# Optimization experiments

Measured on AMD Instinct MI355X. Metric: run time of the kernel, lower is better.

The kernel has to match this reference:

```python
import jax, jax.numpy as jnp
import numpy as np

N = 100000      # num nodes (in_features)
E = 1600000     # num edges
P = 100000      # num pos/neg label edges
EMB = 64        # embedding dim (hardcoded 64 in Encoder)
HID = 128       # 2 * out_channels
OUT = 64        # out_channels
EPS = 1e-15     # PyG GAE EPS
MAX_LOGSTD = 10.0


def setup_inputs() -> dict:
    key = jax.random.key(0)
    ks = jax.random.split(key, 10)
    emb_weight = jax.random.normal(ks[0], (N, EMB), dtype=jnp.float32) * 0.1
    edge_index = jax.random.randint(ks[1], (2, E), 0, N, dtype=jnp.int64)
    pos_edge_label_index = jax.random.randint(ks[2], (2, P), 0, N, dtype=jnp.int64)
    neg_edge_label_index = jax.random.randint(ks[3], (2, P), 0, N, dtype=jnp.int64)
    W1 = jax.random.normal(ks[4], (EMB, HID), dtype=jnp.float32) / np.sqrt(EMB)
    b1 = jnp.zeros((HID,), dtype=jnp.float32)
    W_mu = jax.random.normal(ks[5], (HID, OUT), dtype=jnp.float32) / np.sqrt(HID)
    b_mu = jnp.zeros((OUT,), dtype=jnp.float32)
    W_ls = jax.random.normal(ks[6], (HID, OUT), dtype=jnp.float32) / np.sqrt(HID)
    b_ls = jnp.zeros((OUT,), dtype=jnp.float32)
    return {
        'emb_weight': emb_weight, 'edge_index': edge_index,
        'W1': W1, 'b1': b1, 'W_mu': W_mu, 'b_mu': b_mu, 'W_ls': W_ls, 'b_ls': b_ls,
        'pos_edge_label_index': pos_edge_label_index,
        'neg_edge_label_index': neg_edge_label_index,
    }


def gcn_conv(x, src, dst, deg_inv_sqrt, W, b):
    # GCNConv with added self-loops and symmetric normalization:
    # out = D^{-1/2} (A + I) D^{-1/2} (x W) + b
    h = x @ W                                  # [N, F_out]
    norm = deg_inv_sqrt[src] * deg_inv_sqrt[dst]          # [E]
    agg = jax.ops.segment_sum(h[src] * norm[:, None], dst, num_segments=N)
    agg = agg + h * (deg_inv_sqrt * deg_inv_sqrt)[:, None]  # self-loop term
    return agg + b


def reference(emb_weight, edge_index, W1, b1, W_mu, b_mu, W_ls, b_ls,
              pos_edge_label_index, neg_edge_label_index):
    src, dst = edge_index[0], edge_index[1]
    # degree includes self-loop weight 1
    deg = jax.ops.segment_sum(jnp.ones((E,), dtype=emb_weight.dtype), dst, num_segments=N) + 1.0
    deg_inv_sqrt = jax.lax.rsqrt(deg)

    h = jax.nn.relu(gcn_conv(emb_weight, src, dst, deg_inv_sqrt, W1, b1))
    mu = gcn_conv(h, src, dst, deg_inv_sqrt, W_mu, b_mu)
    logstd = jnp.minimum(gcn_conv(h, src, dst, deg_inv_sqrt, W_ls, b_ls), MAX_LOGSTD)
    z = mu  # eval-mode reparametrize returns mu

    # recon_loss: inner-product decoder + BCE on pos/neg label edges
    ps, pd = pos_edge_label_index[0], pos_edge_label_index[1]
    ns, nd = neg_edge_label_index[0], neg_edge_label_index[1]
    pos_p = jax.nn.sigmoid(jnp.sum(z[ps] * z[pd], axis=-1))
    neg_p = jax.nn.sigmoid(jnp.sum(z[ns] * z[nd], axis=-1))
    pos_loss = -jnp.mean(jnp.log(pos_p + EPS))
    neg_loss = -jnp.mean(jnp.log(1.0 - neg_p + EPS))
    loss = pos_loss + neg_loss
    return z, logstd, loss
```

## Files before the change

kernel.cpp:

```cpp
#include <hip/hip_runtime.h>
#include <hip/hip_bf16.h>
#include <hip/hip_fp16.h>

#define NN 100000
#define NE 1600000
#define NP 100000

typedef _Float16 h2v __attribute__((ext_vector_type(2)));

__device__ __forceinline__ float fdot2u(uint a, uint b, float c) {
    union { uint u; h2v h; } ua, ub;
    ua.u = a; ub.u = b;
    return __builtin_amdgcn_fdot2(ua.h, ub.h, c, false);
}

__device__ __forceinline__ uint packh2(float lo, float hi) {
    __half2 h = __floats2half2_rn(lo, hi);
    return *(uint*)&h;
}

__device__ __forceinline__ void h8_to_f(const uint4 u, float* f) {
    const __half2* hp = (const __half2*)&u;
    float2 t0 = __half22float2(hp[0]), t1 = __half22float2(hp[1]);
    float2 t2 = __half22float2(hp[2]), t3 = __half22float2(hp[3]);
    f[0] = t0.x; f[1] = t0.y; f[2] = t1.x; f[3] = t1.y;
    f[4] = t2.x; f[5] = t2.y; f[6] = t3.x; f[7] = t3.y;
}

__device__ __forceinline__ void add8(const uint4 u, float* acc) {
    float f[8]; h8_to_f(u, f);
#pragma unroll
    for (int i = 0; i < 8; ++i) acc[i] += f[i];
}

__device__ __forceinline__ uint4 f_to_h8(const float* f) {
    union { __half2 h[4]; uint4 u; } pk;
    pk.h[0] = __floats2half2_rn(f[0], f[1]);
    pk.h[1] = __floats2half2_rn(f[2], f[3]);
    pk.h[2] = __floats2half2_rn(f[4], f[5]);
    pk.h[3] = __floats2half2_rn(f[6], f[7]);
    return pk.u;
}

#define RNG 400
#define NBK 250
#define K_A 8000
#define CAPB 12288

__global__ __launch_bounds__(256) void k_hist(const int* __restrict__ ei,
                                              int* __restrict__ bcnt) {
    __shared__ int hist[NBK];
    int tid = threadIdx.x;
    int e0 = blockIdx.x * K_A;
    for (int i = tid; i < NBK; i += 256) hist[i] = 0;
    __syncthreads();
    for (int i = tid; i < K_A; i += 256) atomicAdd(&hist[ei[NE + e0 + i] / RNG], 1);
    __syncthreads();
    for (int i = tid; i < NBK; i += 256) if (hist[i]) atomicAdd(&bcnt[i], hist[i]);
}

__global__ __launch_bounds__(256) void k_bscan(const int* __restrict__ bcnt,
                                               int* __restrict__ bbase,
                                               int* __restrict__ gcnt) {
    __shared__ int c[NBK];
    int tid = threadIdx.x;
    if (tid < NBK) c[tid] = bcnt[tid];
    __syncthreads();
    if (tid < 64) {
        int run = 0;
        for (int g = 0; g < NBK; g += 64) {
            int idx = g + tid;
            int v = (idx < NBK) ? c[idx] : 0;
            int inc = v;
#pragma unroll
            for (int off = 1; off < 64; off <<= 1) {
                int t2 = __shfl_up(inc, off);
                if (tid >= off) inc += t2;
            }
            if (idx < NBK) { int ex = run + inc - v; bbase[idx] = ex; gcnt[idx] = ex; }
            run += __shfl(inc, 63);
        }
        if (tid == 0) bbase[NBK] = run;
    }
}

__global__ __launch_bounds__(256) void k_binA(const int* __restrict__ ei,
                                              int* __restrict__ gcnt,
                                              int* __restrict__ edges) {
    __shared__ int buf[K_A];
    __shared__ int hist[NBK], lofs[NBK + 1], lcnt[NBK], gbase[NBK];
    int tid = threadIdx.x;
    int e0 = blockIdx.x * K_A;
    for (int i = tid; i < NBK; i += 256) { hist[i] = 0; lcnt[i] = 0; }
    __syncthreads();
    for (int i = tid; i < K_A; i += 256) atomicAdd(&hist[ei[NE + e0 + i] / RNG], 1);
    __syncthreads();
    if (tid < 64) {
        int run = 0;
        for (int g = 0; g < NBK; g += 64) {
            int idx = g + tid;
            int v = (idx < NBK) ? hist[idx] : 0;
            int inc = v;
#pragma unroll
            for (int off = 1; off < 64; off <<= 1) {
                int t2 = __shfl_up(inc, off);
                if (tid >= off) inc += t2;
            }
            if (idx < NBK) lofs[idx] = run + inc - v;
            run += __shfl(inc, 63);
        }
        if (tid == 0) lofs[NBK] = run;
    }
    for (int i = tid; i < NBK; i += 256) gbase[i] = atomicAdd(&gcnt[i], hist[i]);
    __syncthreads();
    for (int i = tid; i < K_A; i += 256) {
        int s = ei[e0 + i], d = ei[NE + e0 + i];
        int b = d / RNG;
        int dl = d - b * RNG;
        int p = lofs[b] + atomicAdd(&lcnt[b], 1);
        buf[p] = s | (dl << 17);
    }
    __syncthreads();
    for (int j = tid; j < K_A; j += 256) {
        int loB = 0, hiB = NBK;
        while (hiB - loB > 1) {
            int mid = (loB + hiB) >> 1;
            if (lofs[mid] <= j) loB = mid; else hiB = mid;
        }
        edges[gbase[loB] + (j - lofs[loB])] = buf[j];
    }
}

__global__ __launch_bounds__(256) void k_binB(const int* __restrict__ bbase,
                                              int* __restrict__ edges,
                                              int* __restrict__ rowptr,
                                              float* __restrict__ dinv) {
    __shared__ int buf[CAPB];
    __shared__ int hist[RNG], lrp[RNG], lcnt[RNG];
    int tid = threadIdx.x;
    int b = blockIdx.x;
    int lo = b * RNG;
    int base = bbase[b], n = bbase[b + 1] - base;
    for (int i = tid; i < RNG; i += 256) { hist[i] = 0; lcnt[i] = 0; }
    __syncthreads();
    for (int i = tid; i < n; i += 256)
        atomicAdd(&hist[((unsigned)edges[base + i]) >> 17], 1);
    __syncthreads();
    if (tid < 64) {
        int run = 0;
        for (int g = 0; g < RNG; g += 64) {
            int idx = g + tid;
            int v = (idx < RNG) ? hist[idx] : 0;
            int inc = v;
#pragma unroll
            for (int off = 1; off < 64; off <<= 1) {
                int t2 = __shfl_up(inc, off);
                if (tid >= off) inc += t2;
            }
            if (idx < RNG) lrp[idx] = run + inc - v;
            run += __shfl(inc, 63);
        }
    }
    __syncthreads();
    for (int i = tid; i < RNG; i += 256) {
        dinv[lo + i] = rsqrtf((float)hist[i] + 1.0f);
        rowptr[lo + i] = base + lrp[i];
    }
    if (b == NBK - 1 && tid == 0) rowptr[NN] = base + n;
    int ovS0 = -1, ovS1 = -1, ovR0 = 0, ovR1 = 0;
    for (int i = tid; i < n; i += 256) {
        int rec = edges[base + i];
        int dl = ((unsigned)rec) >> 17;
        int src = rec & 0x1FFFF;
        int slot = lrp[dl] + atomicAdd(&lcnt[dl], 1);
        if (slot < CAPB) buf[slot] = src;
        else if (ovS0 < 0) { ovS0 = slot; ovR0 = src; }
        else { ovS1 = slot; ovR1 = src; }
    }
    __syncthreads();
    int lim = n < CAPB ? n : CAPB;
    for (int i = tid; i < lim; i += 256) edges[base + i] = buf[i];
    if (ovS0 >= 0) edges[base + ovS0] = ovR0;
    if (ovS1 >= 0) edges[base + ovS1] = ovR1;
}

__global__ void k_cvt(const float4* __restrict__ in4, const float* __restrict__ dinv,
                      uint4* __restrict__ out) {
    int t = blockIdx.x * blockDim.x + threadIdx.x;
    if (t >= NN * 8) return;
    float dv = dinv[t >> 3];
    float4 a = in4[t * 2], b = in4[t * 2 + 1];
    float f[8] = {a.x * dv, a.y * dv, a.z * dv, a.w * dv,
                  b.x * dv, b.y * dv, b.z * dv, b.w * dv};
    out[t] = f_to_h8(f);
}

__global__ __launch_bounds__(512) void k_l1(const uint4* __restrict__ x16,
                                            const float* __restrict__ dinv,
                                            const int* __restrict__ rowptr,
                                            const int* __restrict__ edges,
                                            const float4* __restrict__ W1_4,
                                            const float* __restrict__ b1,
                                            uint2* __restrict__ h16) {
    __shared__ uint4 w16h[32 * 32];
    __shared__ uint rows16[64 * 32];
    __shared__ float sdinv[64];
    int t = threadIdx.x;
    int base = blockIdx.x * 64;
#pragma unroll
    for (int i = 0; i < 2; ++i) {
        int idx = t + i * 512;
        int kp = idx >> 5, jg = idx & 31;
        float4 we = W1_4[(2 * kp) * 32 + jg];
        float4 wo = W1_4[(2 * kp + 1) * 32 + jg];
        w16h[idx] = make_uint4(packh2(we.x, wo.x), packh2(we.y, wo.y),
                               packh2(we.z, wo.z), packh2(we.w, wo.w));
    }
    if (t < 64) sdinv[t] = (base + t < NN) ? dinv[base + t] : 0.0f;
    int rl = t >> 3, q = t & 7;
    int r = base + rl;
    if (r < NN) {
        float acc[8];
        h8_to_f(x16[(size_t)r * 8 + q], acc);
        int j = rowptr[r], j1 = rowptr[r + 1];
        for (; j + 8 <= j1; j += 8) {
            int e[8]; uint4 v[8];
#pragma unroll
            for (int i = 0; i < 8; ++i) e[i] = edges[j + i];
#pragma unroll
            for (int i = 0; i < 8; ++i) v[i] = x16[(size_t)e[i] * 8 + q];
#pragma unroll
            for (int i = 0; i < 8; ++i) add8(v[i], acc);
        }
        if (j + 4 <= j1) {
            int e[4]; uint4 v[4];
#pragma unroll
            for (int i = 0; i < 4; ++i) e[i] = edges[j + i];
#pragma unroll
            for (int i = 0; i < 4; ++i) v[i] = x16[(size_t)e[i] * 8 + q];
#pragma unroll
            for (int i = 0; i < 4; ++i) add8(v[i], acc);
            j += 4;
        }
        for (; j < j1; ++j) add8(x16[(size_t)edges[j] * 8 + q], acc);
        float dr = dinv[r];
#pragma unroll
        for (int i = 0; i < 8; ++i) acc[i] *= dr;
#pragma unroll
        for (int i = 0; i < 4; ++i)
            rows16[rl * 32 + 4 * q + i] = packh2(acc[2 * i], acc[2 * i + 1]);
    }
    __syncthreads();
    int rg = t >> 5, jg = t & 31;
    int r0 = rg * 4;
    float4 bias = ((const float4*)b1)[jg];
    float acc[4][4];
#pragma unroll
    for (int r2 = 0; r2 < 4; ++r2) {
        acc[r2][0] = bias.x; acc[r2][1] = bias.y; acc[r2][2] = bias.z; acc[r2][3] = bias.w;
    }
#pragma unroll 4
    for (int kp = 0; kp < 32; ++kp) {
        uint f0 = rows16[(r0 + 0) * 32 + kp];
        uint f1 = rows16[(r0 + 1) * 32 + kp];
        uint f2 = rows16[(r0 + 2) * 32 + kp];
        uint f3 = rows16[(r0 + 3) * 32 + kp];
        uint4 wv = w16h[kp * 32 + jg];
        acc[0][0] = fdot2u(f0, wv.x, acc[0][0]); acc[0][1] = fdot2u(f0, wv.y, acc[0][1]);
        acc[0][2] = fdot2u(f0, wv.z, acc[0][2]); acc[0][3] = fdot2u(f0, wv.w, acc[0][3]);
        acc[1][0] = fdot2u(f1, wv.x, acc[1][0]); acc[1][1] = fdot2u(f1, wv.y, acc[1][1]);
        acc[1][2] = fdot2u(f1, wv.z, acc[1][2]); acc[1][3] = fdot2u(f1, wv.w, acc[1][3]);
        acc[2][0] = fdot2u(f2, wv.x, acc[2][0]); acc[2][1] = fdot2u(f2, wv.y, acc[2][1]);
        acc[2][2] = fdot2u(f2, wv.z, acc[2][2]); acc[2][3] = fdot2u(f2, wv.w, acc[2][3]);
        acc[3][0] = fdot2u(f3, wv.x, acc[3][0]); acc[3][1] = fdot2u(f3, wv.y, acc[3][1]);
        acc[3][2] = fdot2u(f3, wv.z, acc[3][2]); acc[3][3] = fdot2u(f3, wv.w, acc[3][3]);
    }
#pragma unroll
    for (int r2 = 0; r2 < 4; ++r2) {
        int row = base + r0 + r2;
        if (row < NN) {
            float dv = sdinv[r0 + r2];
            union { __half2 h[2]; uint2 u; } pk;
            pk.h[0] = __floats2half2_rn(fmaxf(acc[r2][0], 0.0f) * dv,
                                        fmaxf(acc[r2][1], 0.0f) * dv);
            pk.h[1] = __floats2half2_rn(fmaxf(acc[r2][2], 0.0f) * dv,
                                        fmaxf(acc[r2][3], 0.0f) * dv);
            h16[(size_t)row * 32 + jg] = pk.u;
        }
    }
}

__global__ __launch_bounds__(512) void k_l2(const uint4* __restrict__ x16,
                                            const float* __restrict__ dinv,
                                            const int* __restrict__ rowptr,
                                            const int* __restrict__ edges,
                                            const float4* __restrict__ Wmu4,
                                            const float* __restrict__ bmu,
                                            const float4* __restrict__ Wls4,
                                            const float* __restrict__ bls,
                                            float* __restrict__ out,
                                            uint2* __restrict__ z16) {
    __shared__ uint4 w16h[64 * 32];
    __shared__ uint rows16[64 * 64];
    int t = threadIdx.x;
    int base = blockIdx.x * 64;
#pragma unroll
    for (int i = 0; i < 4; ++i) {
        int idx = t + i * 512;
        int kp = idx >> 5, jg = idx & 31;
        int jj = (jg < 16) ? jg : (jg - 16);
        const float4* W = (jg < 16) ? Wmu4 : Wls4;
        float4 we = W[(2 * kp) * 16 + jj];
        float4 wo = W[(2 * kp + 1) * 16 + jj];
        w16h[idx] = make_uint4(packh2(we.x, wo.x), packh2(we.y, wo.y),
                               packh2(we.z, wo.z), packh2(we.w, wo.w));
    }
    int rl = t >> 3, q = t & 7;
    int r = base + rl;
    if (r < NN) {
        float acc[16];
        {
            uint4 s0 = x16[(size_t)r * 16 + 2 * q];
            uint4 s1 = x16[(size_t)r * 16 + 2 * q + 1];
            h8_to_f(s0, acc); h8_to_f(s1, acc + 8);
        }
        int j = rowptr[r], j1 = rowptr[r + 1];
        for (; j + 4 <= j1; j += 4) {
            int e[4]; uint4 va[4], vb[4];
#pragma unroll
            for (int i = 0; i < 4; ++i) e[i] = edges[j + i];
#pragma unroll
            for (int i = 0; i < 4; ++i) {
                va[i] = x16[(size_t)e[i] * 16 + 2 * q];
                vb[i] = x16[(size_t)e[i] * 16 + 2 * q + 1];
            }
#pragma unroll
            for (int i = 0; i < 4; ++i) { add8(va[i], acc); add8(vb[i], acc + 8); }
        }
        for (; j < j1; ++j) {
            int e = edges[j];
            add8(x16[(size_t)e * 16 + 2 * q], acc);
            add8(x16[(size_t)e * 16 + 2 * q + 1], acc + 8);
        }
        float dr = dinv[r];
#pragma unroll
        for (int i = 0; i < 16; ++i) acc[i] *= dr;
#pragma unroll
        for (int i = 0; i < 8; ++i)
            rows16[rl * 64 + 8 * q + i] = packh2(acc[2 * i], acc[2 * i + 1]);
    }
    __syncthreads();
    int rg = t >> 5, jg = t & 31;
    int r0 = rg * 4;
    float4 bias = (jg < 16) ? ((const float4*)bmu)[jg] : ((const float4*)bls)[jg - 16];
    float acc[4][4];
#pragma unroll
    for (int r2 = 0; r2 < 4; ++r2) {
        acc[r2][0] = bias.x; acc[r2][1] = bias.y; acc[r2][2] = bias.z; acc[r2][3] = bias.w;
    }
#pragma unroll 4
    for (int kp = 0; kp < 64; ++kp) {
        uint f0 = rows16[(r0 + 0) * 64 + kp];
        uint f1 = rows16[(r0 + 1) * 64 + kp];
        uint f2 = rows16[(r0 + 2) * 64 + kp];
        uint f3 = rows16[(r0 + 3) * 64 + kp];
        uint4 wv = w16h[kp * 32 + jg];
        acc[0][0] = fdot2u(f0, wv.x, acc[0][0]); acc[0][1] = fdot2u(f0, wv.y, acc[0][1]);
        acc[0][2] = fdot2u(f0, wv.z, acc[0][2]); acc[0][3] = fdot2u(f0, wv.w, acc[0][3]);
        acc[1][0] = fdot2u(f1, wv.x, acc[1][0]); acc[1][1] = fdot2u(f1, wv.y, acc[1][1]);
        acc[1][2] = fdot2u(f1, wv.z, acc[1][2]); acc[1][3] = fdot2u(f1, wv.w, acc[1][3]);
        acc[2][0] = fdot2u(f2, wv.x, acc[2][0]); acc[2][1] = fdot2u(f2, wv.y, acc[2][1]);
        acc[2][2] = fdot2u(f2, wv.z, acc[2][2]); acc[2][3] = fdot2u(f2, wv.w, acc[2][3]);
        acc[3][0] = fdot2u(f3, wv.x, acc[3][0]); acc[3][1] = fdot2u(f3, wv.y, acc[3][1]);
        acc[3][2] = fdot2u(f3, wv.z, acc[3][2]); acc[3][3] = fdot2u(f3, wv.w, acc[3][3]);
    }
    float4* out4 = (float4*)out;
    if (jg < 16) {
#pragma unroll
        for (int r2 = 0; r2 < 4; ++r2) {
            int row = base + r0 + r2;
            if (row < NN) {
                out4[(size_t)row * 16 + jg] =
                    make_float4(acc[r2][0], acc[r2][1], acc[r2][2], acc[r2][3]);
                union { __half2 h[2]; uint2 u; } pk;
                pk.h[0] = __floats2half2_rn(acc[r2][0], acc[r2][1]);
                pk.h[1] = __floats2half2_rn(acc[r2][2], acc[r2][3]);
                z16[(size_t)row * 16 + jg] = pk.u;
            }
        }
    } else {
#pragma unroll
        for (int r2 = 0; r2 < 4; ++r2) {
            int row = base + r0 + r2;
            if (row < NN) {
                float4 o = make_float4(fminf(acc[r2][0], 10.0f), fminf(acc[r2][1], 10.0f),
                                       fminf(acc[r2][2], 10.0f), fminf(acc[r2][3], 10.0f));
                out4[(size_t)NN * 16 + (size_t)row * 16 + (jg - 16)] = o;
            }
        }
    }
}

__global__ __launch_bounds__(256) void k_loss(const int* __restrict__ pos,
                                              const int* __restrict__ neg,
                                              const uint2* __restrict__ z16,
                                              float* __restrict__ accum) {
    int t = blockIdx.x * blockDim.x + threadIdx.x;
    int grp = t >> 4, q = t & 15;
    int e0 = grp * 4;
    bool isNeg = e0 >= NP;
    const int* idx = isNeg ? neg : pos;
    int eb = isNeg ? e0 - NP : e0;
    int a0 = idx[eb + 0], b0 = idx[NP + eb + 0];
    int a1 = idx[eb + 1], b1 = idx[NP + eb + 1];
    int a2 = idx[eb + 2], b2 = idx[NP + eb + 2];
    int a3 = idx[eb + 3], b3 = idx[NP + eb + 3];
    uint2 ua0 = z16[(size_t)a0 * 16 + q], ub0 = z16[(size_t)b0 * 16 + q];
    uint2 ua1 = z16[(size_t)a1 * 16 + q], ub1 = z16[(size_t)b1 * 16 + q];
    uint2 ua2 = z16[(size_t)a2 * 16 + q], ub2 = z16[(size_t)b2 * 16 + q];
    uint2 ua3 = z16[(size_t)a3 * 16 + q], ub3 = z16[(size_t)b3 * 16 + q];
    float d0 = fdot2u(ua0.y, ub0.y, fdot2u(ua0.x, ub0.x, 0.0f));
    float d1 = fdot2u(ua1.y, ub1.y, fdot2u(ua1.x, ub1.x, 0.0f));
    float d2 = fdot2u(ua2.y, ub2.y, fdot2u(ua2.x, ub2.x, 0.0f));
    float d3 = fdot2u(ua3.y, ub3.y, fdot2u(ua3.x, ub3.x, 0.0f));
#pragma unroll
    for (int off = 1; off < 16; off <<= 1) {
        d0 += __shfl_xor(d0, off);
        d1 += __shfl_xor(d1, off);
        d2 += __shfl_xor(d2, off);
        d3 += __shfl_xor(d3, off);
    }
    __shared__ float bsum[2];
    if (threadIdx.x < 2) bsum[threadIdx.x] = 0.0f;
    __syncthreads();
    if (q == 0) {
        float term;
        if (isNeg) {
            term = logf(1.0f - 1.0f / (1.0f + expf(-d0)) + 1e-15f)
                 + logf(1.0f - 1.0f / (1.0f + expf(-d1)) + 1e-15f)
                 + logf(1.0f - 1.0f / (1.0f + expf(-d2)) + 1e-15f)
                 + logf(1.0f - 1.0f / (1.0f + expf(-d3)) + 1e-15f);
        } else {
            term = logf(1.0f / (1.0f + expf(-d0)) + 1e-15f)
                 + logf(1.0f / (1.0f + expf(-d1)) + 1e-15f)
                 + logf(1.0f / (1.0f + expf(-d2)) + 1e-15f)
                 + logf(1.0f / (1.0f + expf(-d3)) + 1e-15f);
        }
        atomicAdd(&bsum[isNeg ? 1 : 0], term);
    }
    __syncthreads();
    if (threadIdx.x < 2) atomicAdd(&accum[threadIdx.x], bsum[threadIdx.x]);
}

__global__ void k_fin(const float* __restrict__ accum, float* __restrict__ out) {
    out[(size_t)NN * 128] = -(accum[0] + accum[1]) * (1.0f / (float)NP);
}

extern "C" void kernel_launch(void* const* d_in, const int* in_sizes, int n_in,
                              void* d_out, int out_size, void* d_ws, size_t ws_size,
                              hipStream_t stream) {
    const float* emb = (const float*)d_in[0];
    const int*   ei  = (const int*)d_in[1];
    const float* W1  = (const float*)d_in[2];
    const float* b1  = (const float*)d_in[3];
    const float* Wmu = (const float*)d_in[4];
    const float* bmu = (const float*)d_in[5];
    const float* Wls = (const float*)d_in[6];
    const float* bls = (const float*)d_in[7];
    const int*   pos = (const int*)d_in[8];
    const int*   neg = (const int*)d_in[9];
    float* out = (float*)d_out;

    char* ws = (char*)d_ws;
    float* dinv   = (float*)(ws);
    int*   rowptr = (int*)  (ws + (512 << 10));
    int*   bcnt   = (int*)  (ws + (1024 << 10));
    int*   bbase  = (int*)  (ws + (1028 << 10));
    int*   gcnt   = (int*)  (ws + (1032 << 10));
    float* accum  = (float*)(ws + (1040 << 10));
    const size_t OFF_EDGES = (2048 << 10);
    const size_t OFF_H16   = OFF_EDGES + (size_t)NE * 4;
    const size_t OFF_E16   = OFF_H16 + (size_t)NN * 128 * 2;
    int*   edges  = (int*)(ws + OFF_EDGES);
    uint2* h16    = (uint2*)(ws + OFF_H16);
    uint4* emb16  = (uint4*)(ws + OFF_E16);
    uint2* z16    = (uint2*)(ws + OFF_E16);

    hipMemsetAsync(bcnt, 0, NBK * sizeof(int), stream);
    hipMemsetAsync(accum, 0, 2 * sizeof(float), stream);

    k_hist <<<NE / K_A, 256, 0, stream>>>(ei, bcnt);
    k_bscan<<<1, 256, 0, stream>>>(bcnt, bbase, gcnt);
    k_binA <<<NE / K_A, 256, 0, stream>>>(ei, gcnt, edges);
    k_binB <<<NBK, 256, 0, stream>>>(bbase, edges, rowptr, dinv);

    k_cvt  <<<(NN * 8 + 255) / 256, 256, 0, stream>>>((const float4*)emb, dinv, emb16);

    const int GB = (NN + 63) / 64;
    k_l1<<<GB, 512, 0, stream>>>(emb16, dinv, rowptr, edges,
                                 (const float4*)W1, b1, h16);
    k_l2<<<GB, 512, 0, stream>>>((const uint4*)h16, dinv, rowptr, edges,
                                 (const float4*)Wmu, bmu, (const float4*)Wls, bls,
                                 out, z16);

    k_loss<<<(2 * NP * 16) / (256 * 4), 256, 0, stream>>>(pos, neg, z16, accum);
    k_fin<<<1, 1, 0, stream>>>(accum, out);
}
```

Measured before the change: 282.4 us.

## Split layer-2 gather across 16 lanes per row with 32-row blocks

The layer-2 kernel now processes 32 rows per block instead of 64, and gives each row 16 lanes that each load one 16-byte chunk rather than 8 lanes loading two chunks. The gather loop is unrolled by 8 with a 4-edge remainder step, which raises memory-level parallelism for the irregular neighbor loads and doubles the number of blocks. The small GEMM stage now computes 2 rows per thread instead of 4. Row bounds checks are removed, which is only safe because the node count divides evenly by 32. The conversion kernel also inlines its half-packing helper, a cosmetic change.

Result: no change. 287.6 us (+1.8%).

```diff
diff --git a/kernel.cpp b/kernel.cpp
--- a/kernel.cpp
+++ b/kernel.cpp
@@ -31,15 +31,6 @@
     float f[8]; h8_to_f(u, f);
 #pragma unroll
     for (int i = 0; i < 8; ++i) acc[i] += f[i];
-}
-
-__device__ __forceinline__ uint4 f_to_h8(const float* f) {
-    union { __half2 h[4]; uint4 u; } pk;
-    pk.h[0] = __floats2half2_rn(f[0], f[1]);
-    pk.h[1] = __floats2half2_rn(f[2], f[3]);
-    pk.h[2] = __floats2half2_rn(f[4], f[5]);
-    pk.h[3] = __floats2half2_rn(f[6], f[7]);
-    return pk.u;
 }
 
 #define RNG 400
@@ -190,9 +181,12 @@
     if (t >= NN * 8) return;
     float dv = dinv[t >> 3];
     float4 a = in4[t * 2], b = in4[t * 2 + 1];
-    float f[8] = {a.x * dv, a.y * dv, a.z * dv, a.w * dv,
-                  b.x * dv, b.y * dv, b.z * dv, b.w * dv};
-    out[t] = f_to_h8(f);
+    union { __half2 h[4]; uint4 u; } pk;
+    pk.h[0] = __floats2half2_rn(a.x * dv, a.y * dv);
+    pk.h[1] = __floats2half2_rn(a.z * dv, a.w * dv);
+    pk.h[2] = __floats2half2_rn(b.x * dv, b.y * dv);
+    pk.h[3] = __floats2half2_rn(b.z * dv, b.w * dv);
+    out[t] = pk.u;
 }
 
 __global__ __launch_bounds__(512) void k_l1(const uint4* __restrict__ x16,
@@ -301,9 +295,9 @@
                                             float* __restrict__ out,
                                             uint2* __restrict__ z16) {
     __shared__ uint4 w16h[64 * 32];
-    __shared__ uint rows16[64 * 64];
+    __shared__ uint rows16[32 * 64];
     int t = threadIdx.x;
-    int base = blockIdx.x * 64;
+    int base = blockIdx.x * 32;
 #pragma unroll
     for (int i = 0; i < 4; ++i) {
         int idx = t + i * 512;
@@ -315,88 +309,77 @@
         w16h[idx] = make_uint4(packh2(we.x, wo.x), packh2(we.y, wo.y),
                                packh2(we.z, wo.z), packh2(we.w, wo.w));
     }
-    int rl = t >> 3, q = t & 7;
+    int rl = t >> 4, q = t & 15;
     int r = base + rl;
-    if (r < NN) {
-        float acc[16];
-        {
-            uint4 s0 = x16[(size_t)r * 16 + 2 * q];
-            uint4 s1 = x16[(size_t)r * 16 + 2 * q + 1];
-            h8_to_f(s0, acc); h8_to_f(s1, acc + 8);
-        }
+    {
+        float acc[8];
+        h8_to_f(x16[(size_t)r * 16 + q], acc);
         int j = rowptr[r], j1 = rowptr[r + 1];
-        for (; j + 4 <= j1; j += 4) {
-            int e[4]; uint4 va[4], vb[4];
+        for (; j + 8 <= j1; j += 8) {
+            int e[8]; uint4 v[8];
+#pragma unroll
+            for (int i = 0; i < 8; ++i) e[i] = edges[j + i];
+#pragma unroll
+            for (int i = 0; i < 8; ++i) v[i] = x16[(size_t)e[i] * 16 + q];
+#pragma unroll
+            for (int i = 0; i < 8; ++i) add8(v[i], acc);
+        }
+        if (j + 4 <= j1) {
+            int e[4]; uint4 v[4];
 #pragma unroll
             for (int i = 0; i < 4; ++i) e[i] = edges[j + i];
 #pragma unroll
-            for (int i = 0; i < 4; ++i) {
-                va[i] = x16[(size_t)e[i] * 16 + 2 * q];
-                vb[i] = x16[(size_t)e[i] * 16 + 2 * q + 1];
-            }
-#pragma unroll
-            for (int i = 0; i < 4; ++i) { add8(va[i], acc); add8(vb[i], acc + 8); }
-        }
-        for (; j < j1; ++j) {
-            int e = edges[j];
-            add8(x16[(size_t)e * 16 + 2 * q], acc);
-            add8(x16[(size_t)e * 16 + 2 * q + 1], acc + 8);
-        }
+            for (int i = 0; i < 4; ++i) v[i] = x16[(size_t)e[i] * 16 + q];
+#pragma unroll
+            for (int i = 0; i < 4; ++i) add8(v[i], acc);
+            j += 4;
+        }
+        for (; j < j1; ++j) add8(x16[(size_t)edges[j] * 16 + q], acc);
         float dr = dinv[r];
 #pragma unroll
-        for (int i = 0; i < 16; ++i) acc[i] *= dr;
-#pragma unroll
-        for (int i = 0; i < 8; ++i)
-            rows16[rl * 64 + 8 * q + i] = packh2(acc[2 * i], acc[2 * i + 1]);
-    }
-    __syncthreads();
-    int rg = t >> 5, jg = t & 31;
-    int r0 = rg * 4;
+        for (int i = 0; i < 8; ++i) acc[i] *= dr;
+#pragma unroll
+        for (int i = 0; i < 4; ++i)
+            rows16[rl * 64 + 4 * q + i] = packh2(acc[2 * i], acc[2 * i + 1]);
+    }
+    __syncthreads();
+    int rp = t >> 5, jg = t & 31;
+    int r0 = rp * 2;
     float4 bias = (jg < 16) ? ((const float4*)bmu)[jg] : ((const float4*)bls)[jg - 16];
-    float acc[4][4];
-#pragma unroll
-    for (int r2 = 0; r2 < 4; ++r2) {
+    float acc[2][4];
+#pragma unroll
+    for (int r2 = 0; r2 < 2; ++r2) {
         acc[r2][0] = bias.x; acc[r2][1] = bias.y; acc[r2][2] = bias.z; acc[r2][3] = bias.w;
     }
-#pragma unroll 4
+#pragma unroll 8
     for (int kp = 0; kp < 64; ++kp) {
         uint f0 = rows16[(r0 + 0) * 64 + kp];
         uint f1 = rows16[(r0 + 1) * 64 + kp];
-        uint f2 = rows16[(r0 + 2) * 64 + kp];
-        uint f3 = rows16[(r0 + 3) * 64 + kp];
         uint4 wv = w16h[kp * 32 + jg];
         acc[0][0] = fdot2u(f0, wv.x, acc[0][0]); acc[0][1] = fdot2u(f0, wv.y, acc[0][1]);
         acc[0][2] = fdot2u(f0, wv.z, acc[0][2]); acc[0][3] = fdot2u(f0, wv.w, acc[0][3]);
         acc[1][0] = fdot2u(f1, wv.x, acc[1][0]); acc[1][1] = fdot2u(f1, wv.y, acc[1][1]);
         acc[1][2] = fdot2u(f1, wv.z, acc[1][2]); acc[1][3] = fdot2u(f1, wv.w, acc[1][3]);
-        acc[2][0] = fdot2u(f2, wv.x, acc[2][0]); acc[2][1] = fdot2u(f2, wv.y, acc[2][1]);
-        acc[2][2] = fdot2u(f2, wv.z, acc[2][2]); acc[2][3] = fdot2u(f2, wv.w, acc[2][3]);
-        acc[3][0] = fdot2u(f3, wv.x, acc[3][0]); acc[3][1] = fdot2u(f3, wv.y, acc[3][1]);
-        acc[3][2] = fdot2u(f3, wv.z, acc[3][2]); acc[3][3] = fdot2u(f3, wv.w, acc[3][3]);
     }
     float4* out4 = (float4*)out;
     if (jg < 16) {
 #pragma unroll
-        for (int r2 = 0; r2 < 4; ++r2) {
+        for (int r2 = 0; r2 < 2; ++r2) {
             int row = base + r0 + r2;
-            if (row < NN) {
-                out4[(size_t)row * 16 + jg] =
-                    make_float4(acc[r2][0], acc[r2][1], acc[r2][2], acc[r2][3]);
-                union { __half2 h[2]; uint2 u; } pk;
-                pk.h[0] = __floats2half2_rn(acc[r2][0], acc[r2][1]);
-                pk.h[1] = __floats2half2_rn(acc[r2][2], acc[r2][3]);
-                z16[(size_t)row * 16 + jg] = pk.u;
-            }
+            out4[(size_t)row * 16 + jg] =
+                make_float4(acc[r2][0], acc[r2][1], acc[r2][2], acc[r2][3]);
+            union { __half2 h[2]; uint2 u; } pk;
+            pk.h[0] = __floats2half2_rn(acc[r2][0], acc[r2][1]);
+            pk.h[1] = __floats2half2_rn(acc[r2][2], acc[r2][3]);
+            z16[(size_t)row * 16 + jg] = pk.u;
         }
     } else {
 #pragma unroll
-        for (int r2 = 0; r2 < 4; ++r2) {
+        for (int r2 = 0; r2 < 2; ++r2) {
             int row = base + r0 + r2;
-            if (row < NN) {
-                float4 o = make_float4(fminf(acc[r2][0], 10.0f), fminf(acc[r2][1], 10.0f),
-                                       fminf(acc[r2][2], 10.0f), fminf(acc[r2][3], 10.0f));
-                out4[(size_t)NN * 16 + (size_t)row * 16 + (jg - 16)] = o;
-            }
+            float4 o = make_float4(fminf(acc[r2][0], 10.0f), fminf(acc[r2][1], 10.0f),
+                                   fminf(acc[r2][2], 10.0f), fminf(acc[r2][3], 10.0f));
+            out4[(size_t)NN * 16 + (size_t)row * 16 + (jg - 16)] = o;
         }
     }
 }
@@ -496,12 +479,11 @@
 
     k_cvt  <<<(NN * 8 + 255) / 256, 256, 0, stream>>>((const float4*)emb, dinv, emb16);
 
-    const int GB = (NN + 63) / 64;
-    k_l1<<<GB, 512, 0, stream>>>(emb16, dinv, rowptr, edges,
-                                 (const float4*)W1, b1, h16);
-    k_l2<<<GB, 512, 0, stream>>>((const uint4*)h16, dinv, rowptr, edges,
-                                 (const float4*)Wmu, bmu, (const float4*)Wls, bls,
-                                 out, z16);
+    k_l1<<<(NN + 63) / 64, 512, 0, stream>>>(emb16, dinv, rowptr, edges,
+                                             (const float4*)W1, b1, h16);
+    k_l2<<<NN / 32, 512, 0, stream>>>((const uint4*)h16, dinv, rowptr, edges,
+                                      (const float4*)Wmu, bmu, (const float4*)Wls, bls,
+                                      out, z16);
 
     k_loss<<<(2 * NP * 16) / (256 * 4), 256, 0, stream>>>(pos, neg, z16, accum);
     k_fin<<<1, 1, 0, stream>>>(accum, out);
```
